# Optimization experiments

Hardware: AMD Instinct MI355X
Metric: run time of the kernel (lower is better)

Reference implementation:

```python
import jax, jax.numpy as jnp
import numpy as np

EMB = 1024
HEADS = 16
HEAD_DIM = EMB // HEADS
EPS = 1e-5


def gelu_tanh(x):
    c = jnp.sqrt(jnp.asarray(2.0 / jnp.pi, x.dtype))
    return 0.5 * x * (1 + jnp.tanh(c * (x + 0.044715 * x ** 3)))


def layernorm(x, scale, shift):
    mean = jnp.mean(x, axis=-1, keepdims=True)
    var = jnp.mean((x - mean) ** 2, axis=-1, keepdims=True)
    return scale * (x - mean) / jnp.sqrt(var + EPS) + shift


def setup_inputs() -> dict:
    key = jax.random.key(0)
    ks = jax.random.split(key, 12)
    s = 0.02
    x = jax.random.normal(ks[0], (2, 2048, EMB), dtype=jnp.float32)
    Wq = jax.random.normal(ks[1], (EMB, EMB), dtype=jnp.float32) * s
    Wk = jax.random.normal(ks[2], (EMB, EMB), dtype=jnp.float32) * s
    Wv = jax.random.normal(ks[3], (EMB, EMB), dtype=jnp.float32) * s
    Wo = jax.random.normal(ks[4], (EMB, EMB), dtype=jnp.float32) * s
    bo = jnp.zeros((EMB,), jnp.float32)
    W1 = jax.random.normal(ks[5], (EMB, 4 * EMB), dtype=jnp.float32) * s
    b1 = jnp.zeros((4 * EMB,), jnp.float32)
    W2 = jax.random.normal(ks[6], (4 * EMB, EMB), dtype=jnp.float32) * s
    b2 = jnp.zeros((EMB,), jnp.float32)
    g1 = jnp.ones((EMB,), jnp.float32)
    s1 = jnp.zeros((EMB,), jnp.float32)
    g2 = jnp.ones((EMB,), jnp.float32)
    s2 = jnp.zeros((EMB,), jnp.float32)
    return {"x": x, "Wq": Wq, "Wk": Wk, "Wv": Wv, "Wo": Wo, "bo": bo,
            "W1": W1, "b1": b1, "W2": W2, "b2": b2,
            "g1": g1, "s1": s1, "g2": g2, "s2": s2}


def reference(x, Wq, Wk, Wv, Wo, bo, W1, b1, W2, b2, g1, s1, g2, s2):
    B, S, D = x.shape
    # --- attention sub-block (pre-LN) ---
    h = layernorm(x, g1, s1)
    q = (h @ Wq).reshape(B, S, HEADS, HEAD_DIM).transpose(0, 2, 1, 3)
    k = (h @ Wk).reshape(B, S, HEADS, HEAD_DIM).transpose(0, 2, 1, 3)
    v = (h @ Wv).reshape(B, S, HEADS, HEAD_DIM).transpose(0, 2, 1, 3)
    scores = jnp.einsum('bhqd,bhkd->bhqk', q, k) / jnp.sqrt(
        jnp.asarray(HEAD_DIM, x.dtype))
    causal = jnp.triu(jnp.ones((S, S), bool), k=1)
    scores = jnp.where(causal, -jnp.inf, scores)
    attn = jax.nn.softmax(scores, axis=-1)
    ctx = jnp.einsum('bhqk,bhkd->bhqd', attn, v)
    ctx = ctx.transpose(0, 2, 1, 3).reshape(B, S, D)
    x = x + (ctx @ Wo + bo)
    # --- FFN sub-block (pre-LN) ---
    h = layernorm(x, g2, s2)
    h = gelu_tanh(h @ W1 + b1) @ W2 + b2
    return x + h
```

## Files before the change

### kernel.cpp

```cpp
#include <hip/hip_runtime.h>
#include <hip/hip_bf16.h>
#include <math.h>
#include <stdint.h>

typedef __bf16 bf16;
typedef __bf16 bf16x4 __attribute__((ext_vector_type(4)));
typedef __bf16 bf16x8 __attribute__((ext_vector_type(8)));
typedef float f32x4 __attribute__((ext_vector_type(4)));
typedef float f32x16 __attribute__((ext_vector_type(16)));

#define MFMA16(a, b, c) __builtin_amdgcn_mfma_f32_16x16x32_bf16((a), (b), (c), 0, 0, 0)
#define MFMA32(a, b, c) __builtin_amdgcn_mfma_f32_32x32x16_bf16((a), (b), (c), 0, 0, 0)

constexpr int EMB = 1024;
constexpr int SEQ = 2048;
constexpr int BATCH = 2;
constexpr int NTOK = BATCH * SEQ;
constexpr int FFN = 4 * EMB;
constexpr int HEADS = 16;
constexpr int HDIM = 64;

#define QSCALE 0.18033688011112042f

__device__ __forceinline__ void gload16(const void* g, void* l) {
    __builtin_amdgcn_global_load_lds(
        (const __attribute__((address_space(1))) void*)g,
        (__attribute__((address_space(3))) void*)l,
        16, 0, 0);
}

__global__ __launch_bounds__(256) void ln_kernel(const float* __restrict__ x,
                                                 const float* __restrict__ g,
                                                 const float* __restrict__ b,
                                                 bf16* __restrict__ out) {
    int row = blockIdx.x;
    int t = threadIdx.x;
    float4 v = reinterpret_cast<const float4*>(x + (size_t)row * EMB)[t];
    float s = v.x + v.y + v.z + v.w;
    float s2 = v.x * v.x + v.y * v.y + v.z * v.z + v.w * v.w;
#pragma unroll
    for (int o = 1; o < 64; o <<= 1) {
        s += __shfl_xor(s, o);
        s2 += __shfl_xor(s2, o);
    }
    __shared__ float ps[4], ps2[4];
    int w = t >> 6;
    if ((t & 63) == 0) { ps[w] = s; ps2[w] = s2; }
    __syncthreads();
    s = ps[0] + ps[1] + ps[2] + ps[3];
    s2 = ps2[0] + ps2[1] + ps2[2] + ps2[3];
    float mean = s * (1.f / EMB);
    float var = s2 * (1.f / EMB) - mean * mean;
    float rstd = rsqrtf(var + 1e-5f);
    float4 gv = reinterpret_cast<const float4*>(g)[t];
    float4 bv = reinterpret_cast<const float4*>(b)[t];
    bf16* op = out + (size_t)row * EMB + t * 4;
    op[0] = (bf16)(gv.x * (v.x - mean) * rstd + bv.x);
    op[1] = (bf16)(gv.y * (v.y - mean) * rstd + bv.y);
    op[2] = (bf16)(gv.z * (v.z - mean) * rstd + bv.z);
    op[3] = (bf16)(gv.w * (v.w - mean) * rstd + bv.w);
}

__global__ __launch_bounds__(256) void transpose_all(
    const float* __restrict__ Wq, const float* __restrict__ Wk,
    const float* __restrict__ Wv, const float* __restrict__ Wo,
    const float* __restrict__ W1, const float* __restrict__ W2,
    bf16* __restrict__ Wqkvt, bf16* __restrict__ Wot,
    bf16* __restrict__ W1t, bf16* __restrict__ W2t) {
    int b = blockIdx.x;
    const float* W;
    bf16* Wt;
    int K, N, tile;
    if (b < 4096) {
        int w = b >> 10;
        tile = b & 1023;
        W = (w == 0) ? Wq : (w == 1) ? Wk : (w == 2) ? Wv : Wo;
        Wt = (w == 3) ? Wot : Wqkvt + (size_t)w * EMB * EMB;
        K = EMB; N = EMB;
    } else if (b < 8192) {
        tile = b - 4096; W = W1; Wt = W1t; K = EMB; N = FFN;
    } else {
        tile = b - 8192; W = W2; Wt = W2t; K = FFN; N = EMB;
    }
    int ntx = N / 32;
    int n0 = (tile % ntx) * 32, k0 = (tile / ntx) * 32;
    __shared__ float tl[32][33];
    int tx = threadIdx.x & 31, ty = threadIdx.x >> 5;
#pragma unroll
    for (int i = 0; i < 4; i++)
        tl[ty + 8 * i][tx] = W[(size_t)(k0 + ty + 8 * i) * N + n0 + tx];
    __syncthreads();
#pragma unroll
    for (int i = 0; i < 4; i++)
        Wt[(size_t)(n0 + ty + 8 * i) * K + k0 + tx] = (bf16)tl[tx][ty + 8 * i];
}

__global__ __launch_bounds__(256) void vtrans(const bf16* __restrict__ v,
                                              bf16* __restrict__ vt) {
    int bh = blockIdx.y;
    int s0 = blockIdx.x * 64;
    const bf16* src = v + (size_t)bh * SEQ * HDIM + (size_t)s0 * HDIM;
    bf16* dst = vt + (size_t)bh * HDIM * SEQ + s0;
    __shared__ bf16 tile[64][72];
    int t = threadIdx.x;
    int s = t >> 2, d0 = (t & 3) * 16;
    bf16x8 a = *reinterpret_cast<const bf16x8*>(src + s * HDIM + d0);
    bf16x8 b = *reinterpret_cast<const bf16x8*>(src + s * HDIM + d0 + 8);
#pragma unroll
    for (int e = 0; e < 8; e++) {
        tile[d0 + e][s] = a[e];
        tile[d0 + 8 + e][s] = b[e];
    }
    __syncthreads();
    int d = t >> 2, c0 = (t & 3) * 16;
    bf16x8 o0 = *reinterpret_cast<const bf16x8*>(&tile[d][c0]);
    bf16x8 o1 = *reinterpret_cast<const bf16x8*>(&tile[d][c0 + 8]);
    *reinterpret_cast<bf16x8*>(dst + (size_t)d * SEQ + c0) = o0;
    *reinterpret_cast<bf16x8*>(dst + (size_t)d * SEQ + c0 + 8) = o1;
}

template <int MODE>
__global__ __launch_bounds__(512, 1) void gemm8p(const bf16* __restrict__ A,
                                                 const bf16* __restrict__ Bt,
                                                 int K, int N,
                                                 bf16* __restrict__ outB,
                                                 bf16* __restrict__ outB2,
                                                 const float* __restrict__ bias) {
    extern __shared__ char smem[];
    int t = threadIdx.x;
    int wave = t >> 6, lane = t & 63;
    int wr = wave >> 2, wc = wave & 3;
    int lr = lane & 15, lg = lane >> 4;
    int row0 = blockIdx.x * 256;
    int col0 = blockIdx.y * 256;

    int tilesAll = K / 64;
    int nz = gridDim.z, z = blockIdx.z;
    int base = tilesAll / nz, rem = tilesAll - base * nz;
    int myT = base + (z < rem ? 1 : 0);
    int tBeg = z * base + (z < rem ? z : rem);

    const char* aSrc[4];
    const char* bSrc[4];
#pragma unroll
    for (int i = 0; i < 4; i++) {
        int f = t + i * 512;
        int gr = f >> 3, gk = f & 7;
        aSrc[i] = (const char*)A + ((size_t)(row0 + gr) * K + ((gk ^ (gr & 7)) << 3)) * 2
                  + (size_t)tBeg * 128;
        bSrc[i] = (const char*)Bt + ((size_t)(col0 + gr) * K + ((gk ^ (gr & 7)) << 3)) * 2
                  + (size_t)tBeg * 128;
    }

    f32x4 acc[8][4];
#pragma unroll
    for (int m = 0; m < 8; m++)
#pragma unroll
        for (int n = 0; n < 4; n++) acc[m][n] = f32x4{0.f, 0.f, 0.f, 0.f};

#pragma unroll
    for (int i = 0; i < 4; i++) {
        gload16(aSrc[i], smem + (t + i * 512) * 16);
        gload16(bSrc[i], smem + 32768 + (t + i * 512) * 16);
    }
    __syncthreads();

    for (int tk = 0; tk < myT; tk++) {
        int cur = tk & 1;
        const char* la = smem + cur * 65536;
        const char* lb = la + 32768;
        char* na = smem + (cur ^ 1) * 65536;
        bool stage = (tk + 1 < myT);

        bf16x8 bfr[2][4];
#pragma unroll
        for (int ph = 0; ph < 4; ph++) {
            constexpr int PH_KH[4] = {0, 0, 1, 1};
            constexpr int PH_MH[4] = {0, 1, 0, 1};
            const int kh = PH_KH[ph], mh = PH_MH[ph];
            bf16x8 afr[4];
#pragma unroll
            for (int m = 0; m < 4; m++) {
                int row = wr * 128 + (mh * 4 + m) * 16 + lr;
                int gk = kh * 4 + lg;
                afr[m] = *reinterpret_cast<const bf16x8*>(
                    la + row * 128 + ((gk ^ (row & 7)) << 4));
            }
            if (mh == 0) {
#pragma unroll
                for (int n = 0; n < 4; n++) {
                    int row = wc * 64 + n * 16 + lr;
                    int gk = kh * 4 + lg;
                    bfr[kh][n] = *reinterpret_cast<const bf16x8*>(
                        lb + row * 128 + ((gk ^ (row & 7)) << 4));
                }
            }
            if (stage) {
                gload16(aSrc[ph] + 128, na + (t + ph * 512) * 16);
                gload16(bSrc[ph] + 128, na + 32768 + (t + ph * 512) * 16);
            }
            __builtin_amdgcn_s_barrier();
            __builtin_amdgcn_s_setprio(1);
#pragma unroll
            for (int m = 0; m < 4; m++)
#pragma unroll
                for (int n = 0; n < 4; n++)
                    acc[mh * 4 + m][n] = MFMA16(afr[m], bfr[kh][n], acc[mh * 4 + m][n]);
            __builtin_amdgcn_s_setprio(0);
            __builtin_amdgcn_s_barrier();
        }
#pragma unroll
        for (int i = 0; i < 4; i++) { aSrc[i] += 128; bSrc[i] += 128; }
        __syncthreads();
    }

    float bi[4];
    if (MODE == 2) {
#pragma unroll
        for (int n = 0; n < 4; n++) bi[n] = bias[col0 + wc * 64 + n * 16 + lr];
    }
    bf16* pd = outB;
    if (MODE == 3) pd = (z < 2) ? outB + (size_t)z * ((size_t)NTOK * EMB) : outB2;
#pragma unroll
    for (int mf = 0; mf < 8; mf++) {
#pragma unroll
        for (int r = 0; r < 4; r++) {
            int row = row0 + wr * 128 + mf * 16 + 4 * lg + r;
#pragma unroll
            for (int n = 0; n < 4; n++) {
                int col = col0 + wc * 64 + n * 16 + lr;
                float v = acc[mf][n][r];
                if (MODE == 0) {
                    int b_ = row >> 11, s_ = row & 2047;
                    int which = col >> 10, rem_ = col & 1023;
                    int h_ = rem_ >> 6, d_ = rem_ & 63;
                    float sc = (which == 0) ? QSCALE : 1.0f;
                    outB[(size_t)which * (NTOK * EMB) +
                         (((size_t)(b_ * HEADS + h_) * SEQ + s_) << 6) + d_] =
                        (bf16)(v * sc);
                } else if (MODE == 2) {
                    float u = v + bi[n];
                    float gl = 0.5f * u *
                               (1.f + tanhf(0.7978845608028654f *
                                            (u + 0.044715f * u * u * u)));
                    outB[(size_t)row * N + col] = (bf16)gl;
                } else {
                    pd[(size_t)row * N + col] = (bf16)v;
                }
            }
        }
    }
}

__global__ __launch_bounds__(256) void ffn2_reduce(const float* __restrict__ x1,
                                                   const bf16* __restrict__ p01,
                                                   const bf16* __restrict__ p2,
                                                   const float* __restrict__ bias,
                                                   float* __restrict__ out) {
    constexpr int UNITS = NTOK * EMB / 4;
    const bf16* p1 = p01 + (size_t)NTOK * EMB;
    for (int i = blockIdx.x * 256 + threadIdx.x; i < UNITS; i += gridDim.x * 256) {
        float4 r = reinterpret_cast<const float4*>(x1)[i];
        float4 bv = reinterpret_cast<const float4*>(bias)[i & (EMB / 4 - 1)];
        bf16x4 a0 = reinterpret_cast<const bf16x4*>(p01)[i];
        bf16x4 a1 = reinterpret_cast<const bf16x4*>(p1)[i];
        bf16x4 a2 = reinterpret_cast<const bf16x4*>(p2)[i];
        r.x += (float)a0[0] + (float)a1[0] + (float)a2[0] + bv.x;
        r.y += (float)a0[1] + (float)a1[1] + (float)a2[1] + bv.y;
        r.z += (float)a0[2] + (float)a1[2] + (float)a2[2] + bv.z;
        r.w += (float)a0[3] + (float)a1[3] + (float)a2[3] + bv.w;
        reinterpret_cast<float4*>(out)[i] = r;
    }
}

template <int BM, int BN, int BK, int MODE>
__global__ __launch_bounds__(256) void gemm_lds(const bf16* __restrict__ A,
                                                const bf16* __restrict__ Bt,
                                                int M, int N, int K,
                                                float* __restrict__ outF,
                                                bf16* __restrict__ outB,
                                                const float* __restrict__ bias,
                                                const float* __restrict__ resid) {
    constexpr int MR = BM / 32;
    constexpr int NR = BN / 32;
    constexpr int ACH = (BM * BK * 2) / 4096;
    constexpr int BCH = (BN * BK * 2) / 4096;
    __shared__ bf16 sA[BM * BK];
    __shared__ bf16 sB[BN * BK];
    int t = threadIdx.x;
    int wave = t >> 6, lane = t & 63;
    int wr = wave >> 1, wc = wave & 1;
    int lr = lane & 15, lg = lane >> 4;
    int row0 = blockIdx.x * BM;
    int col0 = blockIdx.y * BN;

    const char* aS[ACH];
    const char* bS[BCH];
#pragma unroll
    for (int c = 0; c < ACH; c++) {
        int o = (t + c * 256) * 16;
        aS[c] = (const char*)A + (size_t)(row0 + o / (2 * BK)) * K * 2 + (o & (2 * BK - 1));
    }
#pragma unroll
    for (int c = 0; c < BCH; c++) {
        int o = (t + c * 256) * 16;
        bS[c] = (const char*)Bt + (size_t)(col0 + o / (2 * BK)) * K * 2 + (o & (2 * BK - 1));
    }

    f32x4 acc[MR][NR];
#pragma unroll
    for (int m = 0; m < MR; m++)
#pragma unroll
        for (int n = 0; n < NR; n++) acc[m][n] = f32x4{0.f, 0.f, 0.f, 0.f};

    for (int k0 = 0; k0 < K; k0 += BK) {
        __syncthreads();
#pragma unroll
        for (int c = 0; c < ACH; c++)
            gload16(aS[c], (char*)sA + (t + c * 256) * 16);
#pragma unroll
        for (int c = 0; c < BCH; c++)
            gload16(bS[c], (char*)sB + (t + c * 256) * 16);
#pragma unroll
        for (int c = 0; c < ACH; c++) aS[c] += 2 * BK;
#pragma unroll
        for (int c = 0; c < BCH; c++) bS[c] += 2 * BK;
        __syncthreads();

#pragma unroll
        for (int ks = 0; ks < BK / 32; ks++) {
            bf16x8 a[MR], b[NR];
#pragma unroll
            for (int m = 0; m < MR; m++)
                a[m] = *reinterpret_cast<const bf16x8*>(
                    sA + (wr * (BM / 2) + m * 16 + lr) * BK + ks * 32 + 8 * lg);
#pragma unroll
            for (int n = 0; n < NR; n++)
                b[n] = *reinterpret_cast<const bf16x8*>(
                    sB + (wc * (BN / 2) + n * 16 + lr) * BK + ks * 32 + 8 * lg);
#pragma unroll
            for (int m = 0; m < MR; m++)
#pragma unroll
                for (int n = 0; n < NR; n++)
                    acc[m][n] = MFMA16(a[m], b[n], acc[m][n]);
        }
    }

#pragma unroll
    for (int m = 0; m < MR; m++) {
#pragma unroll
        for (int r = 0; r < 4; r++) {
            int row = row0 + wr * (BM / 2) + m * 16 + 4 * lg + r;
#pragma unroll
            for (int n = 0; n < NR; n++) {
                int col = col0 + wc * (BN / 2) + n * 16 + lr;
                float v = acc[m][n][r];
                size_t idx = (size_t)row * N + col;
                outF[idx] = resid[idx] + v + bias[col];
            }
        }
    }
}

__global__ __launch_bounds__(256, 3) void attn_kernel(const bf16* __restrict__ q,
                                                      const bf16* __restrict__ k,
                                                      const bf16* __restrict__ vt,
                                                      bf16* __restrict__ ctx) {
    int wg = blockIdx.x;
    int wgid = (wg & 7) * 64 + (wg >> 3);
    int bh = wgid >> 4;
    int pair = wgid & 15;
    const bf16* qh = q + (size_t)bh * SEQ * HDIM;
    const bf16* kh = k + (size_t)bh * SEQ * HDIM;
    const bf16* vh = vt + (size_t)bh * HDIM * SEQ;
    int t = threadIdx.x;
    int wave = t >> 6, lane = t & 63;
    int ql = lane & 31, hi = lane >> 5;

    int span = (wave < 2 ? (31 - pair) : pair) * 64;
    int qrow = span + (wave & 1) * 32;
    int myNc = span / 64 + 1;
    int ncAll = 32 - pair;

    __shared__ bf16 sK[2][64 * 64];
    __shared__ bf16 sV[2][64 * 64];
    __shared__ bf16 plds[4][32][72];

    int grow = t >> 3, gg = t & 7;
    const bf16* kSrc0 = kh + (size_t)grow * HDIM + ((gg ^ (grow & 7)) << 3);
    const bf16* kSrc1 = kh + (size_t)(grow + 32) * HDIM + ((gg ^ ((grow + 32) & 7)) << 3);
    const bf16* vSrc0 = vh + (size_t)grow * SEQ + ((gg ^ (grow & 7)) << 3);
    const bf16* vSrc1 = vh + (size_t)(grow + 32) * SEQ + ((gg ^ ((grow + 32) & 7)) << 3);
    char* kD0 = (char*)&sK[0][0] + wave * 1024;
    char* vD0 = (char*)&sV[0][0] + wave * 1024;

    int b_ = bh >> 4, h_ = bh & 15;

    bf16x8 qf[4];
#pragma unroll
    for (int ks = 0; ks < 4; ks++)
        qf[ks] = *reinterpret_cast<const bf16x8*>(
            qh + (size_t)(qrow + ql) * HDIM + ks * 16 + 8 * hi);

    f32x16 o0, o1;
#pragma unroll
    for (int r = 0; r < 16; r++) { o0[r] = 0.f; o1[r] = 0.f; }
    float mx = -1e30f, lsum = 0.f;

    gload16(kSrc0, kD0);
    gload16(kSrc1, kD0 + 4096);
    gload16(vSrc0, vD0);
    gload16(vSrc1, vD0 + 4096);
    __syncthreads();

    for (int c = 0; c < ncAll; c++) {
        int c0 = c * 64;
        if (c + 1 < ncAll) {
            int nb = (c + 1) & 1;
            int cn = c0 + 64;
            gload16(kSrc0 + (size_t)cn * HDIM, kD0 + nb * 8192);
            gload16(kSrc1 + (size_t)cn * HDIM, kD0 + nb * 8192 + 4096);
            gload16(vSrc0 + cn, vD0 + nb * 8192);
            gload16(vSrc1 + cn, vD0 + nb * 8192 + 4096);
        }

        if (c < myNc) {
            const char* kb_ = (const char*)&sK[c & 1][0];
            const char* vb_ = (const char*)&sV[c & 1][0];

            f32x16 st0, st1;
#pragma unroll
            for (int r = 0; r < 16; r++) { st0[r] = 0.f; st1[r] = 0.f; }
#pragma unroll
            for (int ks = 0; ks < 4; ks++) {
                int so = ((2 * ks + hi) ^ (ql & 7)) << 4;
                bf16x8 kA0 = *reinterpret_cast<const bf16x8*>(kb_ + ql * 128 + so);
                bf16x8 kA1 = *reinterpret_cast<const bf16x8*>(kb_ + (32 + ql) * 128 + so);
                st0 = MFMA32(kA0, qf[ks], st0);
                st1 = MFMA32(kA1, qf[ks], st1);
            }

            if (c == myNc - 1) {
#pragma unroll
                for (int r = 0; r < 16; r++) {
                    int kl = c0 + (r & 3) + 8 * (r >> 2) + 4 * hi;
                    if (kl > qrow + ql) st0[r] = -1e30f;
                    if (kl + 32 > qrow + ql) st1[r] = -1e30f;
                }
            }

            float pmax = -1e30f;
#pragma unroll
            for (int r = 0; r < 16; r++)
                pmax = fmaxf(pmax, fmaxf(st0[r], st1[r]));
            pmax = fmaxf(pmax, __shfl_xor(pmax, 32));
            float mn = fmaxf(mx, pmax);
            float scl = __builtin_amdgcn_exp2f(mx - mn);
            mx = mn;
            float ps = 0.f;
#pragma unroll
            for (int j = 0; j < 4; j++) {
                bf16x4 w0, w1;
#pragma unroll
                for (int e = 0; e < 4; e++) {
                    float p0 = __builtin_amdgcn_exp2f(st0[4 * j + e] - mn);
                    float p1 = __builtin_amdgcn_exp2f(st1[4 * j + e] - mn);
                    ps += p0 + p1;
                    w0[e] = (bf16)p0;
                    w1[e] = (bf16)p1;
                }
                *reinterpret_cast<bf16x4*>(&plds[wave][ql][8 * j + 4 * hi]) = w0;
                *reinterpret_cast<bf16x4*>(&plds[wave][ql][32 + 8 * j + 4 * hi]) = w1;
            }
            ps += __shfl_xor(ps, 32);
            lsum = lsum * scl + ps;
#pragma unroll
            for (int r = 0; r < 16; r++) { o0[r] *= scl; o1[r] *= scl; }

#pragma unroll
            for (int ks = 0; ks < 4; ks++) {
                bf16x8 pb = *reinterpret_cast<const bf16x8*>(
                    &plds[wave][ql][ks * 16 + 8 * hi]);
                int so = ((2 * ks + hi) ^ (ql & 7)) << 4;
                bf16x8 vA0 = *reinterpret_cast<const bf16x8*>(vb_ + ql * 128 + so);
                bf16x8 vA1 = *reinterpret_cast<const bf16x8*>(vb_ + (32 + ql) * 128 + so);
                o0 = MFMA32(vA0, pb, o0);
                o1 = MFMA32(vA1, pb, o1);
            }
        }

        __syncthreads();
    }

    float inv = 1.f / lsum;
    size_t base = ((size_t)b_ * SEQ + qrow + ql) * EMB + h_ * HDIM;
#pragma unroll
    for (int j = 0; j < 4; j++) {
        bf16x4 w0, w1;
#pragma unroll
        for (int e = 0; e < 4; e++) {
            w0[e] = (bf16)(o0[4 * j + e] * inv);
            w1[e] = (bf16)(o1[4 * j + e] * inv);
        }
        *reinterpret_cast<bf16x4*>(ctx + base + 8 * j + 4 * hi) = w0;
        *reinterpret_cast<bf16x4*>(ctx + base + 32 + 8 * j + 4 * hi) = w1;
    }
}

extern "C" void kernel_launch(void* const* d_in, const int* in_sizes, int n_in,
                              void* d_out, int out_size, void* d_ws, size_t ws_size,
                              hipStream_t stream) {
    const float* x  = (const float*)d_in[0];
    const float* Wq = (const float*)d_in[1];
    const float* Wk = (const float*)d_in[2];
    const float* Wv = (const float*)d_in[3];
    const float* Wo = (const float*)d_in[4];
    const float* bo = (const float*)d_in[5];
    const float* W1 = (const float*)d_in[6];
    const float* b1 = (const float*)d_in[7];
    const float* W2 = (const float*)d_in[8];
    const float* b2 = (const float*)d_in[9];
    const float* g1 = (const float*)d_in[10];
    const float* s1 = (const float*)d_in[11];
    const float* g2 = (const float*)d_in[12];
    const float* s2 = (const float*)d_in[13];

    const size_t MB = 1ull << 20;
    char* w = (char*)d_ws;
    bf16* Wqkvt = (bf16*)(w + 0 * MB);
    bf16* Wot = (bf16*)(w + 6 * MB);
    bf16* W1t = (bf16*)(w + 8 * MB);
    bf16* W2t = (bf16*)(w + 16 * MB);
    bf16* hbuf = (bf16*)(w + 24 * MB);
    bf16* vtb  = (bf16*)(w + 24 * MB);
    bf16* qkvb = (bf16*)(w + 32 * MB);
    bf16* qb   = (bf16*)(w + 32 * MB);
    bf16* kb   = (bf16*)(w + 40 * MB);
    bf16* vb   = (bf16*)(w + 48 * MB);
    bf16* ctxb = (bf16*)(w + 56 * MB);
    bf16* midb = (bf16*)(w + 32 * MB);
    float* x1  = (float*)(w + 64 * MB);
    bf16* p01  = (bf16*)(w + 0 * MB);
    bf16* p2   = (bf16*)(w + 24 * MB);

    hipFuncSetAttribute(reinterpret_cast<const void*>(gemm8p<0>),
                        hipFuncAttributeMaxDynamicSharedMemorySize, 131072);
    hipFuncSetAttribute(reinterpret_cast<const void*>(gemm8p<2>),
                        hipFuncAttributeMaxDynamicSharedMemorySize, 131072);
    hipFuncSetAttribute(reinterpret_cast<const void*>(gemm8p<3>),
                        hipFuncAttributeMaxDynamicSharedMemorySize, 131072);

    transpose_all<<<dim3(12288), 256, 0, stream>>>(Wq, Wk, Wv, Wo, W1, W2,
                                                   Wqkvt, Wot, W1t, W2t);

    ln_kernel<<<NTOK, 256, 0, stream>>>(x, g1, s1, hbuf);

    gemm8p<0><<<dim3(NTOK / 256, 3072 / 256), 512, 131072, stream>>>(
        hbuf, Wqkvt, EMB, 3072, qkvb, nullptr, nullptr);

    vtrans<<<dim3(SEQ / 64, BATCH * HEADS), 256, 0, stream>>>(vb, vtb);

    attn_kernel<<<dim3(512), 256, 0, stream>>>(qb, kb, vtb, ctxb);

    gemm_lds<128, 64, 32, 1><<<dim3(NTOK / 128, EMB / 64), 256, 0, stream>>>(
        ctxb, Wot, NTOK, EMB, EMB, x1, nullptr, bo, x);

    ln_kernel<<<NTOK, 256, 0, stream>>>(x1, g2, s2, hbuf);

    gemm8p<2><<<dim3(NTOK / 256, FFN / 256), 512, 131072, stream>>>(
        hbuf, W1t, EMB, FFN, midb, nullptr, b1);

    gemm8p<3><<<dim3(NTOK / 256, EMB / 256, 3), 512, 131072, stream>>>(
        midb, W2t, FFN, EMB, p01, p2, nullptr);
    ffn2_reduce<<<dim3(2048), 256, 0, stream>>>(x1, p01, p2, b2, (float*)d_out);
}
```

Before: 246.9 us.

## Split-K out-projection with fused residual+LayerNorm reduce, lazy softmax rescale in attention

The out-projection moves from the small LDS GEMM to the 8-wave gemm8p kernel, split four ways along K into bf16 partials. A new reduce4_ln kernel then adds the residual and bias and applies the second LayerNorm in one pass, replacing the separate ln_kernel launch. The attention kernel now skips the online-softmax rescale of the output accumulators when the new max exceeds the old by no more than 8 (log2 units), uses permlane32_swap instead of shuffles for the cross-half reductions, and XOR-swizzles the P tile in LDS to cut bank conflicts. The risks are lower precision from bf16 split-K partials and larger unnormalized exponentials under the deferred max.

```diff
diff --git a/kernel.cpp b/kernel.cpp
--- a/kernel.cpp
+++ b/kernel.cpp
@@ -8,6 +8,7 @@
 typedef __bf16 bf16x8 __attribute__((ext_vector_type(8)));
 typedef float f32x4 __attribute__((ext_vector_type(4)));
 typedef float f32x16 __attribute__((ext_vector_type(16)));
+typedef unsigned uint2v __attribute__((ext_vector_type(2)));
 
 #define MFMA16(a, b, c) __builtin_amdgcn_mfma_f32_16x16x32_bf16((a), (b), (c), 0, 0, 0)
 #define MFMA32(a, b, c) __builtin_amdgcn_mfma_f32_32x32x16_bf16((a), (b), (c), 0, 0, 0)
@@ -27,6 +28,17 @@
         (const __attribute__((address_space(1))) void*)g,
         (__attribute__((address_space(3))) void*)l,
         16, 0, 0);
+}
+
+__device__ __forceinline__ float xhalf_max(float x) {
+    unsigned u = __float_as_uint(x);
+    uint2v r = __builtin_amdgcn_permlane32_swap(u, u, false, false);
+    return fmaxf(__uint_as_float(r[0]), __uint_as_float(r[1]));
+}
+__device__ __forceinline__ float xhalf_sum(float x) {
+    unsigned u = __float_as_uint(x);
+    uint2v r = __builtin_amdgcn_permlane32_swap(u, u, false, false);
+    return __uint_as_float(r[0]) + __uint_as_float(r[1]);
 }
 
 __global__ __launch_bounds__(256) void ln_kernel(const float* __restrict__ x,
@@ -221,6 +233,7 @@
     }
     bf16* pd = outB;
     if (MODE == 3) pd = (z < 2) ? outB + (size_t)z * ((size_t)NTOK * EMB) : outB2;
+    if (MODE == 4) pd = outB + (size_t)z * ((size_t)NTOK * EMB);
 #pragma unroll
     for (int mf = 0; mf < 8; mf++) {
 #pragma unroll
@@ -252,6 +265,53 @@
     }
 }
 
+__global__ __launch_bounds__(256) void reduce4_ln(const float* __restrict__ x,
+                                                  const bf16* __restrict__ p,
+                                                  const float* __restrict__ bo,
+                                                  const float* __restrict__ g,
+                                                  const float* __restrict__ sh,
+                                                  float* __restrict__ x1,
+                                                  bf16* __restrict__ h2) {
+    int row = blockIdx.x, t = threadIdx.x;
+    size_t i = (size_t)row * 256 + t;
+    float4 v = reinterpret_cast<const float4*>(x)[i];
+    float4 bv = reinterpret_cast<const float4*>(bo)[t];
+    constexpr size_t PSZ = (size_t)NTOK * EMB / 4;
+#pragma unroll
+    for (int k = 0; k < 4; k++) {
+        bf16x4 a = reinterpret_cast<const bf16x4*>(p)[k * PSZ + i];
+        v.x += (float)a[0]; v.y += (float)a[1];
+        v.z += (float)a[2]; v.w += (float)a[3];
+    }
+    v.x += bv.x; v.y += bv.y; v.z += bv.z; v.w += bv.w;
+    reinterpret_cast<float4*>(x1)[i] = v;
+
+    float s = v.x + v.y + v.z + v.w;
+    float s2 = v.x * v.x + v.y * v.y + v.z * v.z + v.w * v.w;
+#pragma unroll
+    for (int o = 1; o < 64; o <<= 1) {
+        s += __shfl_xor(s, o);
+        s2 += __shfl_xor(s2, o);
+    }
+    __shared__ float ps[4], ps2[4];
+    int w = t >> 6;
+    if ((t & 63) == 0) { ps[w] = s; ps2[w] = s2; }
+    __syncthreads();
+    s = ps[0] + ps[1] + ps[2] + ps[3];
+    s2 = ps2[0] + ps2[1] + ps2[2] + ps2[3];
+    float mean = s * (1.f / EMB);
+    float var = s2 * (1.f / EMB) - mean * mean;
+    float rstd = rsqrtf(var + 1e-5f);
+    float4 gv = reinterpret_cast<const float4*>(g)[t];
+    float4 sv = reinterpret_cast<const float4*>(sh)[t];
+    bf16x4 o;
+    o[0] = (bf16)(gv.x * (v.x - mean) * rstd + sv.x);
+    o[1] = (bf16)(gv.y * (v.y - mean) * rstd + sv.y);
+    o[2] = (bf16)(gv.z * (v.z - mean) * rstd + sv.z);
+    o[3] = (bf16)(gv.w * (v.w - mean) * rstd + sv.w);
+    reinterpret_cast<bf16x4*>(h2)[i] = o;
+}
+
 __global__ __launch_bounds__(256) void ffn2_reduce(const float* __restrict__ x1,
                                                    const bf16* __restrict__ p01,
                                                    const bf16* __restrict__ p2,
@@ -273,95 +333,6 @@
     }
 }
 
-template <int BM, int BN, int BK, int MODE>
-__global__ __launch_bounds__(256) void gemm_lds(const bf16* __restrict__ A,
-                                                const bf16* __restrict__ Bt,
-                                                int M, int N, int K,
-                                                float* __restrict__ outF,
-                                                bf16* __restrict__ outB,
-                                                const float* __restrict__ bias,
-                                                const float* __restrict__ resid) {
-    constexpr int MR = BM / 32;
-    constexpr int NR = BN / 32;
-    constexpr int ACH = (BM * BK * 2) / 4096;
-    constexpr int BCH = (BN * BK * 2) / 4096;
-    __shared__ bf16 sA[BM * BK];
-    __shared__ bf16 sB[BN * BK];
-    int t = threadIdx.x;
-    int wave = t >> 6, lane = t & 63;
-    int wr = wave >> 1, wc = wave & 1;
-    int lr = lane & 15, lg = lane >> 4;
-    int row0 = blockIdx.x * BM;
-    int col0 = blockIdx.y * BN;
-
-    const char* aS[ACH];
-    const char* bS[BCH];
-#pragma unroll
-    for (int c = 0; c < ACH; c++) {
-        int o = (t + c * 256) * 16;
-        aS[c] = (const char*)A + (size_t)(row0 + o / (2 * BK)) * K * 2 + (o & (2 * BK - 1));
-    }
-#pragma unroll
-    for (int c = 0; c < BCH; c++) {
-        int o = (t + c * 256) * 16;
-        bS[c] = (const char*)Bt + (size_t)(col0 + o / (2 * BK)) * K * 2 + (o & (2 * BK - 1));
-    }
-
-    f32x4 acc[MR][NR];
-#pragma unroll
-    for (int m = 0; m < MR; m++)
-#pragma unroll
-        for (int n = 0; n < NR; n++) acc[m][n] = f32x4{0.f, 0.f, 0.f, 0.f};
-
-    for (int k0 = 0; k0 < K; k0 += BK) {
-        __syncthreads();
-#pragma unroll
-        for (int c = 0; c < ACH; c++)
-            gload16(aS[c], (char*)sA + (t + c * 256) * 16);
-#pragma unroll
-        for (int c = 0; c < BCH; c++)
-            gload16(bS[c], (char*)sB + (t + c * 256) * 16);
-#pragma unroll
-        for (int c = 0; c < ACH; c++) aS[c] += 2 * BK;
-#pragma unroll
-        for (int c = 0; c < BCH; c++) bS[c] += 2 * BK;
-        __syncthreads();
-
-#pragma unroll
-        for (int ks = 0; ks < BK / 32; ks++) {
-            bf16x8 a[MR], b[NR];
-#pragma unroll
-            for (int m = 0; m < MR; m++)
-                a[m] = *reinterpret_cast<const bf16x8*>(
-                    sA + (wr * (BM / 2) + m * 16 + lr) * BK + ks * 32 + 8 * lg);
-#pragma unroll
-            for (int n = 0; n < NR; n++)
-                b[n] = *reinterpret_cast<const bf16x8*>(
-                    sB + (wc * (BN / 2) + n * 16 + lr) * BK + ks * 32 + 8 * lg);
-#pragma unroll
-            for (int m = 0; m < MR; m++)
-#pragma unroll
-                for (int n = 0; n < NR; n++)
-                    acc[m][n] = MFMA16(a[m], b[n], acc[m][n]);
-        }
-    }
-
-#pragma unroll
-    for (int m = 0; m < MR; m++) {
-#pragma unroll
-        for (int r = 0; r < 4; r++) {
-            int row = row0 + wr * (BM / 2) + m * 16 + 4 * lg + r;
-#pragma unroll
-            for (int n = 0; n < NR; n++) {
-                int col = col0 + wc * (BN / 2) + n * 16 + lr;
-                float v = acc[m][n][r];
-                size_t idx = (size_t)row * N + col;
-                outF[idx] = resid[idx] + v + bias[col];
-            }
-        }
-    }
-}
-
 __global__ __launch_bounds__(256, 3) void attn_kernel(const bf16* __restrict__ q,
                                                       const bf16* __restrict__ k,
                                                       const bf16* __restrict__ vt,
@@ -395,6 +366,8 @@
     char* vD0 = (char*)&sV[0][0] + wave * 1024;
 
     int b_ = bh >> 4, h_ = bh & 15;
+    int vv = 2 * (ql >> 3);
+    char* prow = (char*)&plds[wave][ql][0];
 
     bf16x8 qf[4];
 #pragma unroll
@@ -453,9 +426,10 @@
 #pragma unroll
             for (int r = 0; r < 16; r++)
                 pmax = fmaxf(pmax, fmaxf(st0[r], st1[r]));
-            pmax = fmaxf(pmax, __shfl_xor(pmax, 32));
-            float mn = fmaxf(mx, pmax);
-            float scl = __builtin_amdgcn_exp2f(mx - mn);
+            pmax = xhalf_max(pmax);
+            float mxold = mx;
+            bool defer = (pmax <= mxold + 8.0f);
+            float mn = defer ? mxold : fmaxf(mxold, pmax);
             mx = mn;
             float ps = 0.f;
 #pragma unroll
@@ -469,18 +443,23 @@
                     w0[e] = (bf16)p0;
                     w1[e] = (bf16)p1;
                 }
-                *reinterpret_cast<bf16x4*>(&plds[wave][ql][8 * j + 4 * hi]) = w0;
-                *reinterpret_cast<bf16x4*>(&plds[wave][ql][32 + 8 * j + 4 * hi]) = w1;
-            }
-            ps += __shfl_xor(ps, 32);
-            lsum = lsum * scl + ps;
-#pragma unroll
-            for (int r = 0; r < 16; r++) { o0[r] *= scl; o1[r] *= scl; }
+                *reinterpret_cast<bf16x4*>(prow + (((2 * j + hi) ^ vv) << 3)) = w0;
+                *reinterpret_cast<bf16x4*>(prow + (((8 + 2 * j + hi) ^ vv) << 3)) = w1;
+            }
+            ps = xhalf_sum(ps);
+            if (!__all(defer)) {
+                float scl = __builtin_amdgcn_exp2f(mxold - mn);
+                lsum = lsum * scl + ps;
+#pragma unroll
+                for (int r = 0; r < 16; r++) { o0[r] *= scl; o1[r] *= scl; }
+            } else {
+                lsum += ps;
+            }
 
 #pragma unroll
             for (int ks = 0; ks < 4; ks++) {
                 bf16x8 pb = *reinterpret_cast<const bf16x8*>(
-                    &plds[wave][ql][ks * 16 + 8 * hi]);
+                    prow + (((4 * ks + 2 * hi) ^ vv) << 3));
                 int so = ((2 * ks + hi) ^ (ql & 7)) << 4;
                 bf16x8 vA0 = *reinterpret_cast<const bf16x8*>(vb_ + ql * 128 + so);
                 bf16x8 vA1 = *reinterpret_cast<const bf16x8*>(vb_ + (32 + ql) * 128 + so);
@@ -538,6 +517,8 @@
     bf16* kb   = (bf16*)(w + 40 * MB);
     bf16* vb   = (bf16*)(w + 48 * MB);
     bf16* ctxb = (bf16*)(w + 56 * MB);
+    bf16* wop  = (bf16*)(w + 24 * MB);
+    bf16* h2   = (bf16*)(w + 0 * MB);
     bf16* midb = (bf16*)(w + 32 * MB);
     float* x1  = (float*)(w + 64 * MB);
     bf16* p01  = (bf16*)(w + 0 * MB);
@@ -549,6 +530,8 @@
                         hipFuncAttributeMaxDynamicSharedMemorySize, 131072);
     hipFuncSetAttribute(reinterpret_cast<const void*>(gemm8p<3>),
                         hipFuncAttributeMaxDynamicSharedMemorySize, 131072);
+    hipFuncSetAttribute(reinterpret_cast<const void*>(gemm8p<4>),
+                        hipFuncAttributeMaxDynamicSharedMemorySize, 131072);
 
     transpose_all<<<dim3(12288), 256, 0, stream>>>(Wq, Wk, Wv, Wo, W1, W2,
                                                    Wqkvt, Wot, W1t, W2t);
@@ -562,13 +545,13 @@
 
     attn_kernel<<<dim3(512), 256, 0, stream>>>(qb, kb, vtb, ctxb);
 
-    gemm_lds<128, 64, 32, 1><<<dim3(NTOK / 128, EMB / 64), 256, 0, stream>>>(
-        ctxb, Wot, NTOK, EMB, EMB, x1, nullptr, bo, x);
-
-    ln_kernel<<<NTOK, 256, 0, stream>>>(x1, g2, s2, hbuf);
+    gemm8p<4><<<dim3(NTOK / 256, EMB / 256, 4), 512, 131072, stream>>>(
+        ctxb, Wot, EMB, EMB, wop, nullptr, nullptr);
+
+    reduce4_ln<<<NTOK, 256, 0, stream>>>(x, wop, bo, g2, s2, x1, h2);
 
     gemm8p<2><<<dim3(NTOK / 256, FFN / 256), 512, 131072, stream>>>(
-        hbuf, W1t, EMB, FFN, midb, nullptr, b1);
+        h2, W1t, EMB, FFN, midb, nullptr, b1);
 
     gemm8p<3><<<dim3(NTOK / 256, EMB / 256, 3), 512, 131072, stream>>>(
         midb, W2t, FFN, EMB, p01, p2, nullptr);
```

Result: no change. 249.6 us (+1.1%).

## Keep attention probabilities in registers via permlane32 swap and defer rescaling

Applied to the files above, without the earlier changes.

The flash-attention inner loop no longer writes the softmax probabilities to a per-wave LDS buffer and reads them back. Instead it packs them to bf16 in registers and rearranges them across the two half-waves with permlane32_swap to form the MFMA B operand. The cross-half max and sum reductions also use permlane32_swap instead of shuffles. It adds a lazy rescale: the running max is only updated, and the accumulators only rescaled, when the new block max exceeds the old by more than 8 in log2 units. This saves LDS traffic and multiplies at the cost of more complex register shuffling and a small bounded overflow risk.

```diff
diff --git a/kernel.cpp b/kernel.cpp
--- a/kernel.cpp
+++ b/kernel.cpp
@@ -4,10 +4,13 @@
 #include <stdint.h>
 
 typedef __bf16 bf16;
+typedef __bf16 bf16x2 __attribute__((ext_vector_type(2)));
 typedef __bf16 bf16x4 __attribute__((ext_vector_type(4)));
 typedef __bf16 bf16x8 __attribute__((ext_vector_type(8)));
 typedef float f32x4 __attribute__((ext_vector_type(4)));
 typedef float f32x16 __attribute__((ext_vector_type(16)));
+typedef unsigned uint2v __attribute__((ext_vector_type(2)));
+typedef unsigned uint4v __attribute__((ext_vector_type(4)));
 
 #define MFMA16(a, b, c) __builtin_amdgcn_mfma_f32_16x16x32_bf16((a), (b), (c), 0, 0, 0)
 #define MFMA32(a, b, c) __builtin_amdgcn_mfma_f32_32x32x16_bf16((a), (b), (c), 0, 0, 0)
@@ -27,6 +30,24 @@
         (const __attribute__((address_space(1))) void*)g,
         (__attribute__((address_space(3))) void*)l,
         16, 0, 0);
+}
+
+__device__ __forceinline__ float xhalf_max(float x) {
+    unsigned u = __float_as_uint(x);
+    uint2v r = __builtin_amdgcn_permlane32_swap(u, u, false, false);
+    return fmaxf(__uint_as_float(r[0]), __uint_as_float(r[1]));
+}
+__device__ __forceinline__ float xhalf_sum(float x) {
+    unsigned u = __float_as_uint(x);
+    uint2v r = __builtin_amdgcn_permlane32_swap(u, u, false, false);
+    return __uint_as_float(r[0]) + __uint_as_float(r[1]);
+}
+
+__device__ __forceinline__ unsigned pkbf(float a, float b) {
+    bf16x2 v;
+    v[0] = (bf16)a;
+    v[1] = (bf16)b;
+    return __builtin_bit_cast(unsigned, v);
 }
 
 __global__ __launch_bounds__(256) void ln_kernel(const float* __restrict__ x,
@@ -384,7 +405,6 @@
 
     __shared__ bf16 sK[2][64 * 64];
     __shared__ bf16 sV[2][64 * 64];
-    __shared__ bf16 plds[4][32][72];
 
     int grow = t >> 3, gg = t & 7;
     const bf16* kSrc0 = kh + (size_t)grow * HDIM + ((gg ^ (grow & 7)) << 3);
@@ -453,39 +473,53 @@
 #pragma unroll
             for (int r = 0; r < 16; r++)
                 pmax = fmaxf(pmax, fmaxf(st0[r], st1[r]));
-            pmax = fmaxf(pmax, __shfl_xor(pmax, 32));
-            float mn = fmaxf(mx, pmax);
-            float scl = __builtin_amdgcn_exp2f(mx - mn);
+            pmax = xhalf_max(pmax);
+            float mxold = mx;
+            bool defer = (pmax <= mxold + 8.0f);
+            float mn = defer ? mxold : fmaxf(mxold, pmax);
             mx = mn;
             float ps = 0.f;
 #pragma unroll
-            for (int j = 0; j < 4; j++) {
-                bf16x4 w0, w1;
-#pragma unroll
-                for (int e = 0; e < 4; e++) {
-                    float p0 = __builtin_amdgcn_exp2f(st0[4 * j + e] - mn);
-                    float p1 = __builtin_amdgcn_exp2f(st1[4 * j + e] - mn);
-                    ps += p0 + p1;
-                    w0[e] = (bf16)p0;
-                    w1[e] = (bf16)p1;
+            for (int r = 0; r < 16; r++) {
+                st0[r] = __builtin_amdgcn_exp2f(st0[r] - mn);
+                st1[r] = __builtin_amdgcn_exp2f(st1[r] - mn);
+                ps += st0[r] + st1[r];
+            }
+            ps = xhalf_sum(ps);
+            if (!__all(defer)) {
+                float scl = __builtin_amdgcn_exp2f(mxold - mn);
+                lsum = lsum * scl + ps;
+#pragma unroll
+                for (int r = 0; r < 16; r++) { o0[r] *= scl; o1[r] *= scl; }
+            } else {
+                lsum += ps;
+            }
+
+#pragma unroll
+            for (int h2 = 0; h2 < 2; h2++) {
+                f32x16 P = h2 ? st1 : st0;
+#pragma unroll
+                for (int sub = 0; sub < 2; sub++) {
+                    int ks = 2 * h2 + sub;
+                    int bs = 8 * sub;
+                    unsigned X0 = pkbf(P[bs + 0], P[bs + 1]);
+                    unsigned X1 = pkbf(P[bs + 2], P[bs + 3]);
+                    unsigned Y0 = pkbf(P[bs + 4], P[bs + 5]);
+                    unsigned Y1 = pkbf(P[bs + 6], P[bs + 7]);
+                    uint2v s0 = __builtin_amdgcn_permlane32_swap(X0, Y0, false, false);
+                    uint2v s1 = __builtin_amdgcn_permlane32_swap(X1, Y1, false, false);
+                    uint4v uw;
+                    uw[0] = s0[0];
+                    uw[1] = s1[0];
+                    uw[2] = s0[1];
+                    uw[3] = s1[1];
+                    bf16x8 pb = __builtin_bit_cast(bf16x8, uw);
+                    int so = ((2 * ks + hi) ^ (ql & 7)) << 4;
+                    bf16x8 vA0 = *reinterpret_cast<const bf16x8*>(vb_ + ql * 128 + so);
+                    bf16x8 vA1 = *reinterpret_cast<const bf16x8*>(vb_ + (32 + ql) * 128 + so);
+                    o0 = MFMA32(vA0, pb, o0);
+                    o1 = MFMA32(vA1, pb, o1);
                 }
-                *reinterpret_cast<bf16x4*>(&plds[wave][ql][8 * j + 4 * hi]) = w0;
-                *reinterpret_cast<bf16x4*>(&plds[wave][ql][32 + 8 * j + 4 * hi]) = w1;
-            }
-            ps += __shfl_xor(ps, 32);
-            lsum = lsum * scl + ps;
-#pragma unroll
-            for (int r = 0; r < 16; r++) { o0[r] *= scl; o1[r] *= scl; }
-
-#pragma unroll
-            for (int ks = 0; ks < 4; ks++) {
-                bf16x8 pb = *reinterpret_cast<const bf16x8*>(
-                    &plds[wave][ql][ks * 16 + 8 * hi]);
-                int so = ((2 * ks + hi) ^ (ql & 7)) << 4;
-                bf16x8 vA0 = *reinterpret_cast<const bf16x8*>(vb_ + ql * 128 + so);
-                bf16x8 vA1 = *reinterpret_cast<const bf16x8*>(vb_ + (32 + ql) * 128 + so);
-                o0 = MFMA32(vA0, pb, o0);
-                o1 = MFMA32(vA1, pb, o1);
             }
         }
 
```

Result: no change. 243.5 us (-1.4%).
